# Optimization experiments

Measured on AMD Instinct MI355X. Metric: run time of the kernel, lower is better.

Reference implementation:

```python
import jax, jax.numpy as jnp
import numpy as np

IMG_H, IMG_W = 800, 800
OUT_H, OUT_W = 7, 7
SR = 2  # sampling_ratio (exact sampling branch)
SCALES = (0.25, 0.125, 0.0625, 0.03125)
CANONICAL_SCALE = 224.0
CANONICAL_LEVEL = 4.0
K_MIN, K_MAX = 2, 5  # -log2(0.25), -log2(1/32)
EPS = 1e-6


def _prep_coords(c, size):
    # c: continuous coords (K, N); returns low/high int indices and lerp weights
    c = jnp.maximum(c, 0.0)
    lo = c.astype(jnp.int32)  # truncation == floor for c >= 0
    at_edge = lo >= size - 1
    hi = jnp.where(at_edge, size - 1, lo + 1)
    lo = jnp.where(at_edge, size - 1, lo)
    l = c - lo.astype(c.dtype)
    return lo, hi, l, 1.0 - l


def roi_align_exact(feat, batch_idx, rois, scale):
    # feat: (B, C, H, W); batch_idx: (K,) int; rois: (K, 4) xyxy; exact sampling, aligned=False
    B, C, H, W = feat.shape
    x1 = rois[:, 0] * scale
    y1 = rois[:, 1] * scale
    x2 = rois[:, 2] * scale
    y2 = rois[:, 3] * scale
    roi_w = jnp.maximum(x2 - x1, 1.0)
    roi_h = jnp.maximum(y2 - y1, 1.0)
    bin_h = roi_h / OUT_H
    bin_w = roi_w / OUT_W
    ph = jnp.arange(OUT_H, dtype=feat.dtype)
    pw = jnp.arange(OUT_W, dtype=feat.dtype)
    iy = jnp.arange(SR, dtype=feat.dtype)
    ix = jnp.arange(SR, dtype=feat.dtype)
    # (K, OUT_H, SR) -> (K, OUT_H*SR)
    y = y1[:, None, None] + ph[None, :, None] * bin_h[:, None, None] + (iy[None, None, :] + 0.5) * (bin_h / SR)[:, None, None]
    x = x1[:, None, None] + pw[None, :, None] * bin_w[:, None, None] + (ix[None, None, :] + 0.5) * (bin_w / SR)[:, None, None]
    K = rois.shape[0]
    NY, NX = OUT_H * SR, OUT_W * SR
    y = y.reshape(K, NY)
    x = x.reshape(K, NX)
    y_lo, y_hi, ly, hy = _prep_coords(y, H)
    x_lo, x_hi, lx, hx = _prep_coords(x, W)

    b = batch_idx[:, None, None]

    def gather(yi, xi):
        # -> (K, NY, NX, C): advanced indices around ':' put (K,NY,NX) in front
        return feat[b, :, yi[:, :, None], xi[:, None, :]]

    val = (hy[:, :, None, None] * hx[:, None, :, None] * gather(y_lo, x_lo)
           + hy[:, :, None, None] * lx[:, None, :, None] * gather(y_lo, x_hi)
           + ly[:, :, None, None] * hx[:, None, :, None] * gather(y_hi, x_lo)
           + ly[:, :, None, None] * lx[:, None, :, None] * gather(y_hi, x_hi))
    # (K, OUT_H, SR, OUT_W, SR, C) -> sum sampling grid, avg by count
    val = val.reshape(K, OUT_H, SR, OUT_W, SR, C).sum(axis=(2, 4)) / float(SR * SR)
    return jnp.transpose(val, (0, 3, 1, 2))  # (K, C, OUT_H, OUT_W)


def multiscale_roi_align(feats, boxes):
    B, L, _ = boxes.shape
    K = B * L
    rois = boxes.reshape(K, 4)
    batch_idx = jnp.repeat(jnp.arange(B, dtype=jnp.int32), L)
    area = (rois[:, 2] - rois[:, 0]) * (rois[:, 3] - rois[:, 1])
    s = jnp.sqrt(area)
    lvl = jnp.floor(CANONICAL_LEVEL + jnp.log2(s / CANONICAL_SCALE) + EPS)
    levels = jnp.clip(lvl, K_MIN, K_MAX).astype(jnp.int32) - K_MIN
    C = feats[0].shape[1]
    out = jnp.zeros((K, C, OUT_H, OUT_W), dtype=feats[0].dtype)
    for l, (f, sc) in enumerate(zip(feats, SCALES)):
        pooled = roi_align_exact(f, batch_idx, rois, sc)
        out = out + jnp.where((levels == l)[:, None, None, None], pooled, 0.0)
    return out


def setup_inputs() -> dict:
    key = jax.random.key(0)
    k0, k1, k2, k3, kw, kh, kx, ky = jax.random.split(key, 8)
    B, C, L = 2, 256, 256
    feat0 = jax.random.normal(k0, (B, C, 200, 200), dtype=jnp.float32)
    feat1 = jax.random.normal(k1, (B, C, 100, 100), dtype=jnp.float32)
    feat2 = jax.random.normal(k2, (B, C, 50, 50), dtype=jnp.float32)
    feat3 = jax.random.normal(k3, (B, C, 25, 25), dtype=jnp.float32)
    w = jax.random.uniform(kw, (B, L), minval=16.0, maxval=512.0)
    h = jax.random.uniform(kh, (B, L), minval=16.0, maxval=512.0)
    x1 = jax.random.uniform(kx, (B, L)) * (IMG_W - w)
    y1 = jax.random.uniform(ky, (B, L)) * (IMG_H - h)
    boxes = jnp.stack([x1, y1, x1 + w, y1 + h], axis=-1).astype(jnp.float32)
    return {"feat0": feat0, "feat1": feat1, "feat2": feat2, "feat3": feat3, "boxes": boxes}


def reference(feat0, feat1, feat2, feat3, boxes):
    return multiscale_roi_align([feat0, feat1, feat2, feat3], boxes)
```

## Files before the change

kernel.cpp:

```cpp
#include <hip/hip_runtime.h>


#define OUT_HW 7
#define KROIS 512
#define NCH 256
#define LPB 256

__global__ __launch_bounds__(256) void msroi_kernel(
    const float* __restrict__ f0, const float* __restrict__ f1,
    const float* __restrict__ f2, const float* __restrict__ f3,
    const float* __restrict__ boxes, float* __restrict__ out, int total)
{
    int idx = blockIdx.x * blockDim.x + threadIdx.x;
    if (idx >= total) return;

    int pw = idx % OUT_HW;
    int ph = (idx / OUT_HW) % OUT_HW;
    int c  = (idx / (OUT_HW * OUT_HW)) % NCH;
    int k  = idx / (OUT_HW * OUT_HW * NCH);
    int b  = k / LPB;

    float bx1 = boxes[k * 4 + 0];
    float by1 = boxes[k * 4 + 1];
    float bx2 = boxes[k * 4 + 2];
    float by2 = boxes[k * 4 + 3];

    float area = (bx2 - bx1) * (by2 - by1);
    float s = sqrtf(area);
    float lvlf = floorf(4.0f + log2f(s * (1.0f / 224.0f)) + 1e-6f);
    lvlf = fminf(fmaxf(lvlf, 2.0f), 5.0f);
    int lvl = (int)lvlf - 2;

    const float* feat;
    int H, W;
    float scale;
    if (lvl == 0)      { feat = f0; H = 200; W = 200; scale = 0.25f;    }
    else if (lvl == 1) { feat = f1; H = 100; W = 100; scale = 0.125f;   }
    else if (lvl == 2) { feat = f2; H = 50;  W = 50;  scale = 0.0625f;  }
    else               { feat = f3; H = 25;  W = 25;  scale = 0.03125f; }

    float x1 = bx1 * scale;
    float y1 = by1 * scale;
    float x2 = bx2 * scale;
    float y2 = by2 * scale;
    float roi_w = fmaxf(x2 - x1, 1.0f);
    float roi_h = fmaxf(y2 - y1, 1.0f);
    float bin_h = roi_h * (1.0f / OUT_HW);
    float bin_w = roi_w * (1.0f / OUT_HW);

    const float* base = feat + ((size_t)b * NCH + c) * (size_t)(H * W);

    float acc = 0.0f;
#pragma unroll
    for (int iy = 0; iy < 2; ++iy) {
        float y = y1 + ph * bin_h + (iy + 0.5f) * (bin_h * 0.5f);
        y = fmaxf(y, 0.0f);
        int ylo = (int)y;
        int yhi;
        if (ylo >= H - 1) { ylo = H - 1; yhi = H - 1; }
        else              { yhi = ylo + 1; }
        float ly = y - (float)ylo;
        float hy = 1.0f - ly;
#pragma unroll
        for (int ix = 0; ix < 2; ++ix) {
            float x = x1 + pw * bin_w + (ix + 0.5f) * (bin_w * 0.5f);
            x = fmaxf(x, 0.0f);
            int xlo = (int)x;
            int xhi;
            if (xlo >= W - 1) { xlo = W - 1; xhi = W - 1; }
            else              { xhi = xlo + 1; }
            float lx = x - (float)xlo;
            float hx = 1.0f - lx;

            float v00 = base[ylo * W + xlo];
            float v01 = base[ylo * W + xhi];
            float v10 = base[yhi * W + xlo];
            float v11 = base[yhi * W + xhi];

            acc += hy * hx * v00 + hy * lx * v01 + ly * hx * v10 + ly * lx * v11;
        }
    }
    out[idx] = acc * 0.25f;
}

extern "C" void kernel_launch(void* const* d_in, const int* in_sizes, int n_in,
                              void* d_out, int out_size, void* d_ws, size_t ws_size,
                              hipStream_t stream)
{
    const float* f0 = (const float*)d_in[0];
    const float* f1 = (const float*)d_in[1];
    const float* f2 = (const float*)d_in[2];
    const float* f3 = (const float*)d_in[3];
    const float* boxes = (const float*)d_in[4];
    float* out = (float*)d_out;

    int total = KROIS * NCH * OUT_HW * OUT_HW;
    int block = 256;
    int grid = (total + block - 1) / block;
    msroi_kernel<<<grid, block, 0, stream>>>(f0, f1, f2, f3, boxes, out, total);
}
```

Before: 210.4 us.

## Stage ROI feature patches in LDS per block of ROI and channels

Restructures the kernel so each block handles one ROI and four channels. The block first copies the ROI's bounding patch from global memory into shared memory with coalesced row loads, then computes the bilinear samples from LDS using sample indices and weights that are precomputed once per block. This replaces many scattered, uncoalesced global gathers. The cost is an extra full-patch load and a barrier, and only 196 of 256 threads do compute. The patch buffer is fixed at 1024 floats per channel, which assumes patches never exceed that size.

```diff
diff --git a/kernel.cpp b/kernel.cpp
--- a/kernel.cpp
+++ b/kernel.cpp
@@ -2,34 +2,34 @@
 
 
 #define OUT_HW 7
-#define KROIS 512
 #define NCH 256
-#define LPB 256
+#define CC 4
+#define PATCH_MAX 1024
 
-__global__ __launch_bounds__(256) void msroi_kernel(
+__global__ __launch_bounds__(256) void msroi_lds_kernel(
     const float* __restrict__ f0, const float* __restrict__ f1,
     const float* __restrict__ f2, const float* __restrict__ f3,
-    const float* __restrict__ boxes, float* __restrict__ out, int total)
+    const float* __restrict__ boxes, float* __restrict__ out)
 {
-    int idx = blockIdx.x * blockDim.x + threadIdx.x;
-    if (idx >= total) return;
+    const int tid = threadIdx.x;
+    const int k  = blockIdx.y;
+    const int c0 = blockIdx.x * CC;
+    const int b  = k >> 8;
 
-    int pw = idx % OUT_HW;
-    int ph = (idx / OUT_HW) % OUT_HW;
-    int c  = (idx / (OUT_HW * OUT_HW)) % NCH;
-    int k  = idx / (OUT_HW * OUT_HW * NCH);
-    int b  = k / LPB;
+    __shared__ float s_patch[CC * PATCH_MAX];
+    __shared__ int   s_xlo[14], s_xhi[14], s_ylo[14], s_yhi[14];
+    __shared__ float s_lx[14], s_ly[14];
 
-    float bx1 = boxes[k * 4 + 0];
-    float by1 = boxes[k * 4 + 1];
-    float bx2 = boxes[k * 4 + 2];
-    float by2 = boxes[k * 4 + 3];
+    const float bx1 = boxes[k * 4 + 0];
+    const float by1 = boxes[k * 4 + 1];
+    const float bx2 = boxes[k * 4 + 2];
+    const float by2 = boxes[k * 4 + 3];
 
-    float area = (bx2 - bx1) * (by2 - by1);
-    float s = sqrtf(area);
+    const float area = (bx2 - bx1) * (by2 - by1);
+    const float s = sqrtf(area);
     float lvlf = floorf(4.0f + log2f(s * (1.0f / 224.0f)) + 1e-6f);
     lvlf = fminf(fmaxf(lvlf, 2.0f), 5.0f);
-    int lvl = (int)lvlf - 2;
+    const int lvl = (int)lvlf - 2;
 
     const float* feat;
     int H, W;
@@ -39,48 +39,100 @@
     else if (lvl == 2) { feat = f2; H = 50;  W = 50;  scale = 0.0625f;  }
     else               { feat = f3; H = 25;  W = 25;  scale = 0.03125f; }
 
-    float x1 = bx1 * scale;
-    float y1 = by1 * scale;
-    float x2 = bx2 * scale;
-    float y2 = by2 * scale;
-    float roi_w = fmaxf(x2 - x1, 1.0f);
-    float roi_h = fmaxf(y2 - y1, 1.0f);
-    float bin_h = roi_h * (1.0f / OUT_HW);
-    float bin_w = roi_w * (1.0f / OUT_HW);
+    const float x1 = bx1 * scale;
+    const float y1 = by1 * scale;
+    const float roi_w = fmaxf(bx2 * scale - x1, 1.0f);
+    const float roi_h = fmaxf(by2 * scale - y1, 1.0f);
+    const float bin_w = roi_w * (1.0f / OUT_HW);
+    const float bin_h = roi_h * (1.0f / OUT_HW);
 
-    const float* base = feat + ((size_t)b * NCH + c) * (size_t)(H * W);
+    auto prep_lo = [](float c, int size) {
+        float cm = fmaxf(c, 0.0f);
+        int lo = (int)cm;
+        return (lo >= size - 1) ? (size - 1) : lo;
+    };
+    auto prep_hi = [](float c, int size) {
+        float cm = fmaxf(c, 0.0f);
+        int lo = (int)cm;
+        return (lo >= size - 1) ? (size - 1) : (lo + 1);
+    };
+    const int px0 = prep_lo(x1 + 0.25f * bin_w, W);
+    const int px1 = prep_hi(x1 + 6.75f * bin_w, W);
+    const int py0 = prep_lo(y1 + 0.25f * bin_h, H);
+    const int py1 = prep_hi(y1 + 6.75f * bin_h, H);
+    const int pw_cnt = px1 - px0 + 1;
+    const int ph_cnt = py1 - py0 + 1;
 
-    float acc = 0.0f;
+    if (tid < 14) {
+        float x = x1 + ((float)tid * 0.5f + 0.25f) * bin_w;
+        float cm = fmaxf(x, 0.0f);
+        int lo = (int)cm;
+        int hi;
+        if (lo >= W - 1) { lo = W - 1; hi = W - 1; }
+        else             { hi = lo + 1; }
+        s_xlo[tid] = lo - px0;
+        s_xhi[tid] = hi - px0;
+        s_lx[tid]  = cm - (float)lo;
+    } else if (tid >= 32 && tid < 46) {
+        int i = tid - 32;
+        float y = y1 + ((float)i * 0.5f + 0.25f) * bin_h;
+        float cm = fmaxf(y, 0.0f);
+        int lo = (int)cm;
+        int hi;
+        if (lo >= H - 1) { lo = H - 1; hi = H - 1; }
+        else             { hi = lo + 1; }
+        s_ylo[i] = lo - py0;
+        s_yhi[i] = hi - py0;
+        s_ly[i]  = cm - (float)lo;
+    }
+
+    const int tx = tid & 31;
+    const int ty = tid >> 5;
+    const size_t HW = (size_t)H * W;
+    const size_t bc = (size_t)b * NCH + c0;
+    const int rows_total = CC * ph_cnt;
+
+    for (int rr = ty; rr < rows_total; rr += 8) {
+        int cl = (rr >= ph_cnt) + (rr >= 2 * ph_cnt) + (rr >= 3 * ph_cnt);
+        int r = rr - cl * ph_cnt;
+        const float* src = feat + (bc + cl) * HW + (size_t)(py0 + r) * W + px0;
+        float* dst = &s_patch[cl * PATCH_MAX + r * pw_cnt];
+        for (int col = tx; col < pw_cnt; col += 32)
+            dst[col] = src[col];
+    }
+    __syncthreads();
+
+    if (tid < CC * 49) {
+        const int cl  = tid / 49;
+        const int pix = tid % 49;
+        const int ph  = pix / 7;
+        const int pw  = pix % 7;
+
+        float acc = 0.0f;
+        const float* patch = &s_patch[cl * PATCH_MAX];
 #pragma unroll
-    for (int iy = 0; iy < 2; ++iy) {
-        float y = y1 + ph * bin_h + (iy + 0.5f) * (bin_h * 0.5f);
-        y = fmaxf(y, 0.0f);
-        int ylo = (int)y;
-        int yhi;
-        if (ylo >= H - 1) { ylo = H - 1; yhi = H - 1; }
-        else              { yhi = ylo + 1; }
-        float ly = y - (float)ylo;
-        float hy = 1.0f - ly;
+        for (int iy = 0; iy < 2; ++iy) {
+            const int sy = ph * 2 + iy;
+            const int r0 = s_ylo[sy] * pw_cnt;
+            const int r1 = s_yhi[sy] * pw_cnt;
+            const float ly = s_ly[sy];
+            const float hy = 1.0f - ly;
 #pragma unroll
-        for (int ix = 0; ix < 2; ++ix) {
-            float x = x1 + pw * bin_w + (ix + 0.5f) * (bin_w * 0.5f);
-            x = fmaxf(x, 0.0f);
-            int xlo = (int)x;
-            int xhi;
-            if (xlo >= W - 1) { xlo = W - 1; xhi = W - 1; }
-            else              { xhi = xlo + 1; }
-            float lx = x - (float)xlo;
-            float hx = 1.0f - lx;
-
-            float v00 = base[ylo * W + xlo];
-            float v01 = base[ylo * W + xhi];
-            float v10 = base[yhi * W + xlo];
-            float v11 = base[yhi * W + xhi];
-
-            acc += hy * hx * v00 + hy * lx * v01 + ly * hx * v10 + ly * lx * v11;
+            for (int ix = 0; ix < 2; ++ix) {
+                const int sx = pw * 2 + ix;
+                const int xlo = s_xlo[sx];
+                const int xhi = s_xhi[sx];
+                const float lx = s_lx[sx];
+                const float hx = 1.0f - lx;
+                const float v00 = patch[r0 + xlo];
+                const float v01 = patch[r0 + xhi];
+                const float v10 = patch[r1 + xlo];
+                const float v11 = patch[r1 + xhi];
+                acc += hy * hx * v00 + hy * lx * v01 + ly * hx * v10 + ly * lx * v11;
+            }
         }
+        out[((size_t)k * NCH + c0) * 49 + tid] = acc * 0.25f;
     }
-    out[idx] = acc * 0.25f;
 }
 
 extern "C" void kernel_launch(void* const* d_in, const int* in_sizes, int n_in,
@@ -94,8 +146,7 @@
     const float* boxes = (const float*)d_in[4];
     float* out = (float*)d_out;
 
-    int total = KROIS * NCH * OUT_HW * OUT_HW;
-    int block = 256;
-    int grid = (total + block - 1) / block;
-    msroi_kernel<<<grid, block, 0, stream>>>(f0, f1, f2, f3, boxes, out, total);
+    dim3 grid(NCH / CC, 512, 1);
+    dim3 block(256, 1, 1);
+    msroi_lds_kernel<<<grid, block, 0, stream>>>(f0, f1, f2, f3, boxes, out);
 }
```

Result: slower. 262.6 us (+24.8%).

## Stage ROI feature patches in shared memory per channel group and precompute taps

Applied to the files above, without the earlier changes.

Reorganises the kernel so each block handles one ROI and 8 channels. The block first copies the dense bounding patch of the ROI into LDS, then computes the bilinear samples from shared memory. A separate setup kernel precomputes per-ROI level, patch extents and tap offsets and weights into workspace. This is meant to cut redundant scattered global gathers and repeated per-thread box maths, at the cost of an extra launch, a block-wide sync and a fixed LDS patch size that assumes ROI patches fit in PM entries.

```diff
diff --git a/kernel.cpp b/kernel.cpp
--- a/kernel.cpp
+++ b/kernel.cpp
@@ -2,85 +2,180 @@
 
 
 #define OUT_HW 7
-#define KROIS 512
 #define NCH 256
-#define LPB 256
-
-__global__ __launch_bounds__(256) void msroi_kernel(
+#define CC 8
+#define PM 1152
+#define WSTRIDE 80
+#define NROI 512
+#define THREADS 512
+
+
+__device__ __forceinline__ void roi_scalars(const float* __restrict__ boxes, int k,
+    int& lvl, int& H, int& W, float& x1, float& y1, float& bin_w, float& bin_h,
+    int& px0, int& py0, int& pw_cnt, int& ph_cnt)
+{
+    float bx1 = boxes[k*4+0], by1 = boxes[k*4+1], bx2 = boxes[k*4+2], by2 = boxes[k*4+3];
+    float area = (bx2-bx1)*(by2-by1);
+    float s = sqrtf(area);
+    float lvlf = floorf(4.0f + log2f(s*(1.0f/224.0f)) + 1e-6f);
+    lvlf = fminf(fmaxf(lvlf, 2.0f), 5.0f);
+    lvl = (int)lvlf - 2;
+    float scale;
+    if (lvl == 0)      { H=200; W=200; scale=0.25f;    }
+    else if (lvl == 1) { H=100; W=100; scale=0.125f;   }
+    else if (lvl == 2) { H=50;  W=50;  scale=0.0625f;  }
+    else               { H=25;  W=25;  scale=0.03125f; }
+    x1 = bx1*scale; y1 = by1*scale;
+    float roi_w = fmaxf(bx2*scale - x1, 1.0f);
+    float roi_h = fmaxf(by2*scale - y1, 1.0f);
+    bin_w = roi_w*(1.0f/7.0f); bin_h = roi_h*(1.0f/7.0f);
+    float c; int lo;
+    c = fmaxf(x1 + 0.25f*bin_w, 0.0f); lo = (int)c; px0 = (lo >= W-1) ? (W-1) : lo;
+    c = fmaxf(x1 + 6.75f*bin_w, 0.0f); lo = (int)c; int px1e = (lo >= W-1) ? (W-1) : (lo+1);
+    c = fmaxf(y1 + 0.25f*bin_h, 0.0f); lo = (int)c; py0 = (lo >= H-1) ? (H-1) : lo;
+    c = fmaxf(y1 + 6.75f*bin_h, 0.0f); lo = (int)c; int py1e = (lo >= H-1) ? (H-1) : (lo+1);
+    pw_cnt = px1e - px0 + 1;
+    ph_cnt = py1e - py0 + 1;
+}
+
+__global__ __launch_bounds__(64) void roi_setup(const float* __restrict__ boxes,
+                                                int* __restrict__ ws)
+{
+    int k = blockIdx.x*64 + threadIdx.x;
+    if (k >= NROI) return;
+    int lvl, H, W, px0, py0, pw_cnt, ph_cnt;
+    float x1, y1, bin_w, bin_h;
+    roi_scalars(boxes, k, lvl, H, W, x1, y1, bin_w, bin_h, px0, py0, pw_cnt, ph_cnt);
+    int pw_pad = (pw_cnt + 1) | 1;
+    int* p = ws + k*WSTRIDE;
+    p[0]=lvl; p[1]=px0; p[2]=py0; p[3]=pw_cnt; p[4]=pw_pad;
+    p[5]=pw_cnt*ph_cnt; p[6]=W; p[7]=H*W; p[8]=ph_cnt;
+    for (int i = 0; i < 14; ++i) {
+        float c = fmaxf(x1 + ((float)i*0.5f + 0.25f)*bin_w, 0.0f);
+        int lo = (int)c; int xle; float lx;
+        if (lo >= W-1) { xle = (W-1) - px0; lx = 0.0f; }
+        else           { xle = lo - px0;    lx = c - (float)lo; }
+        p[16+i] = xle;
+        p[30+i] = __float_as_int(lx);
+    }
+    for (int i = 0; i < 14; ++i) {
+        float c = fmaxf(y1 + ((float)i*0.5f + 0.25f)*bin_h, 0.0f);
+        int lo = (int)c; int r; float ly;
+        if (lo >= H-1) { r = (H-1) - py0; ly = 0.0f; }
+        else           { r = lo - py0;    ly = c - (float)lo; }
+        p[44+i] = r*pw_pad;
+        p[58+i] = __float_as_int(ly);
+    }
+}
+
+template<bool USE_WS>
+__global__ __launch_bounds__(THREADS) void msroi_main(
     const float* __restrict__ f0, const float* __restrict__ f1,
     const float* __restrict__ f2, const float* __restrict__ f3,
-    const float* __restrict__ boxes, float* __restrict__ out, int total)
-{
-    int idx = blockIdx.x * blockDim.x + threadIdx.x;
-    if (idx >= total) return;
-
-    int pw = idx % OUT_HW;
-    int ph = (idx / OUT_HW) % OUT_HW;
-    int c  = (idx / (OUT_HW * OUT_HW)) % NCH;
-    int k  = idx / (OUT_HW * OUT_HW * NCH);
-    int b  = k / LPB;
-
-    float bx1 = boxes[k * 4 + 0];
-    float by1 = boxes[k * 4 + 1];
-    float bx2 = boxes[k * 4 + 2];
-    float by2 = boxes[k * 4 + 3];
-
-    float area = (bx2 - bx1) * (by2 - by1);
-    float s = sqrtf(area);
-    float lvlf = floorf(4.0f + log2f(s * (1.0f / 224.0f)) + 1e-6f);
-    lvlf = fminf(fmaxf(lvlf, 2.0f), 5.0f);
-    int lvl = (int)lvlf - 2;
-
-    const float* feat;
-    int H, W;
-    float scale;
-    if (lvl == 0)      { feat = f0; H = 200; W = 200; scale = 0.25f;    }
-    else if (lvl == 1) { feat = f1; H = 100; W = 100; scale = 0.125f;   }
-    else if (lvl == 2) { feat = f2; H = 50;  W = 50;  scale = 0.0625f;  }
-    else               { feat = f3; H = 25;  W = 25;  scale = 0.03125f; }
-
-    float x1 = bx1 * scale;
-    float y1 = by1 * scale;
-    float x2 = bx2 * scale;
-    float y2 = by2 * scale;
-    float roi_w = fmaxf(x2 - x1, 1.0f);
-    float roi_h = fmaxf(y2 - y1, 1.0f);
-    float bin_h = roi_h * (1.0f / OUT_HW);
-    float bin_w = roi_w * (1.0f / OUT_HW);
-
-    const float* base = feat + ((size_t)b * NCH + c) * (size_t)(H * W);
-
-    float acc = 0.0f;
+    const float* __restrict__ boxes, const int* __restrict__ ws,
+    float* __restrict__ out)
+{
+    __shared__ float s_patch[CC*PM];
+    __shared__ int   s_taps[56];
+
+    const int tid = threadIdx.x;
+    const int k  = blockIdx.y;
+    const int c0 = blockIdx.x * CC;
+
+    int lvl, px0, py0, pw_cnt, pw_pad, pdense, W, HW, ph_cnt;
+    if constexpr (USE_WS) {
+        const int* p = ws + k*WSTRIDE;
+        lvl = p[0]; px0 = p[1]; py0 = p[2]; pw_cnt = p[3]; pw_pad = p[4];
+        pdense = p[5]; W = p[6]; HW = p[7]; ph_cnt = p[8];
+        if (tid < 56) s_taps[tid] = p[16 + tid];
+    } else {
+        int H; float x1, y1, bin_w, bin_h;
+        roi_scalars(boxes, k, lvl, H, W, x1, y1, bin_w, bin_h, px0, py0, pw_cnt, ph_cnt);
+        pw_pad = (pw_cnt + 1) | 1; pdense = pw_cnt*ph_cnt; HW = H*W;
+        if (tid < 14) {
+            float c = fmaxf(x1 + ((float)tid*0.5f + 0.25f)*bin_w, 0.0f);
+            int lo = (int)c; int xle; float lx;
+            if (lo >= W-1) { xle = (W-1) - px0; lx = 0.0f; }
+            else           { xle = lo - px0;    lx = c - (float)lo; }
+            s_taps[tid] = xle; s_taps[14+tid] = __float_as_int(lx);
+        } else if (tid >= 64 && tid < 78) {
+            int i = tid - 64;
+            float c = fmaxf(y1 + ((float)i*0.5f + 0.25f)*bin_h, 0.0f);
+            int lo = (int)c; int r; float ly;
+            if (lo >= H-1) { r = (H-1) - py0; ly = 0.0f; }
+            else           { r = lo - py0;    ly = c - (float)lo; }
+            s_taps[28+i] = r*pw_pad; s_taps[42+i] = __float_as_int(ly);
+        }
+    }
+
+    const float* feat = (lvl == 0) ? f0 : (lvl == 1) ? f1 : (lvl == 2) ? f2 : f3;
+    const int b = k >> 8;
+    const float* bp = feat + (size_t)(b*NCH + c0) * (size_t)HW;
+
+    int nz = ph_cnt + 1 + pw_cnt;
+    for (int z = tid; z < nz; z += THREADS) {
+        int wi = (z <= ph_cnt) ? (z*pw_pad + pw_cnt)
+                               : (ph_cnt*pw_pad + (z - (ph_cnt + 1)));
 #pragma unroll
-    for (int iy = 0; iy < 2; ++iy) {
-        float y = y1 + ph * bin_h + (iy + 0.5f) * (bin_h * 0.5f);
-        y = fmaxf(y, 0.0f);
-        int ylo = (int)y;
-        int yhi;
-        if (ylo >= H - 1) { ylo = H - 1; yhi = H - 1; }
-        else              { yhi = ylo + 1; }
-        float ly = y - (float)ylo;
-        float hy = 1.0f - ly;
+        for (int j = 0; j < CC; ++j) s_patch[j*PM + wi] = 0.0f;
+    }
+
+    float inv_pw = 1.0f / (float)pw_cnt;
+    for (int i = tid; i < pdense; i += THREADS) {
+        int r = (int)((float)i * inv_pw);
+        int col = i - r*pw_cnt;
+        if (col < 0)             { col += pw_cnt; --r; }
+        else if (col >= pw_cnt)  { col -= pw_cnt; ++r; }
+        int go = (py0 + r)*W + (px0 + col);
+        int wi = r*pw_pad + col;
 #pragma unroll
-        for (int ix = 0; ix < 2; ++ix) {
-            float x = x1 + pw * bin_w + (ix + 0.5f) * (bin_w * 0.5f);
-            x = fmaxf(x, 0.0f);
-            int xlo = (int)x;
-            int xhi;
-            if (xlo >= W - 1) { xlo = W - 1; xhi = W - 1; }
-            else              { xhi = xlo + 1; }
-            float lx = x - (float)xlo;
-            float hx = 1.0f - lx;
-
-            float v00 = base[ylo * W + xlo];
-            float v01 = base[ylo * W + xhi];
-            float v10 = base[yhi * W + xlo];
-            float v11 = base[yhi * W + xhi];
-
-            acc += hy * hx * v00 + hy * lx * v01 + ly * hx * v10 + ly * lx * v11;
-        }
-    }
-    out[idx] = acc * 0.25f;
+        for (int j = 0; j < CC; ++j)
+            s_patch[j*PM + wi] = bp[(size_t)j*(size_t)HW + (size_t)go];
+    }
+    __syncthreads();
+
+    if (tid < CC*49) {
+        int cl = tid / 49, pix = tid - cl*49;
+        int ph = pix / 7,  pw  = pix - ph*7;
+        int cb = cl*PM;
+        int xl0 = s_taps[2*pw]   + cb;
+        int xl1 = s_taps[2*pw+1] + cb;
+        float lx0 = __int_as_float(s_taps[14 + 2*pw]);
+        float lx1 = __int_as_float(s_taps[15 + 2*pw]);
+        int r00 = s_taps[28 + 2*ph];
+        int r01 = s_taps[29 + 2*ph];
+        float ly0 = __int_as_float(s_taps[42 + 2*ph]);
+        float ly1 = __int_as_float(s_taps[43 + 2*ph]);
+        float hx0 = 1.0f - lx0, hx1 = 1.0f - lx1;
+        float hy0 = 1.0f - ly0, hy1 = 1.0f - ly1;
+
+        float acc = 0.0f;
+        {
+            int a = r00 + xl0, a2 = a + pw_pad;
+            float v00 = s_patch[a], v01 = s_patch[a+1];
+            float v10 = s_patch[a2], v11 = s_patch[a2+1];
+            acc += hy0*(hx0*v00 + lx0*v01) + ly0*(hx0*v10 + lx0*v11);
+        }
+        {
+            int a = r00 + xl1, a2 = a + pw_pad;
+            float v00 = s_patch[a], v01 = s_patch[a+1];
+            float v10 = s_patch[a2], v11 = s_patch[a2+1];
+            acc += hy0*(hx1*v00 + lx1*v01) + ly0*(hx1*v10 + lx1*v11);
+        }
+        {
+            int a = r01 + xl0, a2 = a + pw_pad;
+            float v00 = s_patch[a], v01 = s_patch[a+1];
+            float v10 = s_patch[a2], v11 = s_patch[a2+1];
+            acc += hy1*(hx0*v00 + lx0*v01) + ly1*(hx0*v10 + lx0*v11);
+        }
+        {
+            int a = r01 + xl1, a2 = a + pw_pad;
+            float v00 = s_patch[a], v01 = s_patch[a+1];
+            float v10 = s_patch[a2], v11 = s_patch[a2+1];
+            acc += hy1*(hx1*v00 + lx1*v01) + ly1*(hx1*v10 + lx1*v11);
+        }
+        out[((size_t)k*NCH + c0)*49 + tid] = acc * 0.25f;
+    }
 }
 
 extern "C" void kernel_launch(void* const* d_in, const int* in_sizes, int n_in,
@@ -94,8 +189,16 @@
     const float* boxes = (const float*)d_in[4];
     float* out = (float*)d_out;
 
-    int total = KROIS * NCH * OUT_HW * OUT_HW;
-    int block = 256;
-    int grid = (total + block - 1) / block;
-    msroi_kernel<<<grid, block, 0, stream>>>(f0, f1, f2, f3, boxes, out, total);
-}
+    dim3 grid(NCH / CC, NROI, 1);
+    dim3 block(THREADS, 1, 1);
+    size_t need = (size_t)NROI * WSTRIDE * sizeof(int);
+
+    if (d_ws != nullptr && ws_size >= need) {
+        roi_setup<<<dim3((NROI + 63)/64), dim3(64), 0, stream>>>(boxes, (int*)d_ws);
+        msroi_main<true><<<grid, block, 0, stream>>>(f0, f1, f2, f3, boxes,
+                                                     (const int*)d_ws, out);
+    } else {
+        msroi_main<false><<<grid, block, 0, stream>>>(f0, f1, f2, f3, boxes,
+                                                      nullptr, out);
+    }
+}
```

Measured after the change: 176.9 us. -15.9%, faster.
